# Performance work log

Measured on AMD Instinct MI355X. Metric: run time of the kernel, lower is better.

The kernel has to match this reference:

```python
import jax, jax.numpy as jnp
import numpy as np

EPS = 1e-12  # torch F.normalize eps


def setup_inputs() -> dict:
    key = jax.random.key(0)
    k1, k2, k3 = jax.random.split(key, 3)
    B, C, N, E, EMB = 128, 16, 128, 4, 16
    OUT = EMB // E  # Linear(emb_sz, emb_sz // num_edges)
    x = jax.random.normal(k1, (B, C, N, EMB), dtype=jnp.float32)
    A = jax.random.uniform(k2, (E, N, N), dtype=jnp.float32)  # non-negative adjacency
    # per-edge-type Linear weights, stored [E, in, out] so y = x @ W[e]
    W = jax.random.normal(k3, (E, EMB, OUT), dtype=jnp.float32) * (1.0 / np.sqrt(EMB))
    return {"x": x, "A": A, "W": W}


def reference(x, A, W):
    # F.normalize(A[e], dim=0): L2-normalize each column -> norm over rows (axis=1 of [E,N,N])
    col_norm = jnp.sqrt(jnp.sum(A * A, axis=1, keepdims=True))  # [E,1,N]
    An = A / jnp.maximum(col_norm, EPS)                         # [E,N,N]
    # x.transpose(3,2) @ An[e] then transpose back:
    # out[e,b,c,m,f] = sum_n x[b,c,n,f] * An[e,n,m]
    msg = jnp.einsum('bcnf,enm->ebcmf', x, An)                  # [E,B,C,N,EMB]
    # per-edge Linear (bias=False) + relu
    h = jax.nn.relu(jnp.einsum('ebcmf,efo->ebcmo', msg, W))     # [E,B,C,N,OUT]
    E_, B, C, N, O = h.shape
    # torch.cat([h_0, h_1, ...], axis=1) -> [B, E*C, N, OUT]
    out = jnp.transpose(h, (1, 0, 2, 3, 4)).reshape(B, E_ * C, N, O)
    return out
```

## Files before the change

### kernel.cpp

```cpp
#include <hip/hip_runtime.h>
#include <math.h>

#define EPSN 1e-12f

typedef __attribute__((ext_vector_type(8))) __bf16 bf16x8;
typedef __attribute__((ext_vector_type(8))) short short8;
typedef __attribute__((ext_vector_type(4))) float floatx4;

static __device__ __forceinline__ unsigned short f2bf(float f) {
    return __builtin_bit_cast(unsigned short, (__bf16)f);
}

__global__ __launch_bounds__(256)
void prep_kernel(const float* __restrict__ A, unsigned short* __restrict__ At) {
    __shared__ float Asub[128][33];
    __shared__ float red[8][32];
    __shared__ float rnv[32];
    const int t  = threadIdx.x;
    const int e  = blockIdx.x >> 2;
    const int m0 = (blockIdx.x & 3) * 32;
    const float* Ae = A + e * 16384 + m0;

    #pragma unroll
    for (int i = 0; i < 16; ++i) {
        int idx = t + i * 256;
        int n = idx >> 5, ml = idx & 31;
        Asub[n][ml] = Ae[n * 128 + ml];
    }
    __syncthreads();
    {
        int ml = t & 31, g = t >> 5;
        float s = 0.f;
        #pragma unroll
        for (int j = 0; j < 16; ++j) {
            float v = Asub[g * 16 + j][ml];
            s += v * v;
        }
        red[g][ml] = s;
    }
    __syncthreads();
    if (t < 32) {
        float s = 0.f;
        #pragma unroll
        for (int g = 0; g < 8; ++g) s += red[g][t];
        rnv[t] = 1.0f / fmaxf(sqrtf(s), EPSN);
    }
    __syncthreads();
    {
        int ml = t >> 3;
        int n0 = (t & 7) * 16;
        float r = rnv[ml];
        unsigned short hs[16];
        #pragma unroll
        for (int j = 0; j < 16; ++j)
            hs[j] = f2bf(Asub[n0 + j][ml] * r);
        uint4* dst = (uint4*)(At + ((size_t)(e * 128 + m0 + ml) * 128 + n0));
        dst[0] = *(const uint4*)&hs[0];
        dst[1] = *(const uint4*)&hs[8];
    }
}

__global__ __launch_bounds__(256, 4)
void gcn_mfma_kernel(const float* __restrict__ x, const float* __restrict__ W,
                     const unsigned short* __restrict__ At,
                     float* __restrict__ out) {
    __shared__ __align__(16) unsigned char xw[32768];

    const int t   = threadIdx.x;
    const int gid = blockIdx.x;
    const int h   = gid >> 8;
    const int bc0 = (gid & 255) * 8;

    float4 xf[4][4];
    #pragma unroll
    for (int p = 0; p < 4; ++p) {
        int pair = p * 256 + t;
        int bcl = pair >> 7, n = pair & 127;
        const float4* xp = (const float4*)(x + ((size_t)(bc0 + bcl) * 128 + n) * 16);
        xf[p][0] = xp[0]; xf[p][1] = xp[1]; xf[p][2] = xp[2]; xf[p][3] = xp[3];
    }
    const int nn = t & 127;
    #pragma unroll 1
    for (int e = 0; e < 4; ++e) {
        float4 We[16];
        const float4* wp = (const float4*)(W + e * 64);
        #pragma unroll
        for (int f = 0; f < 16; ++f) We[f] = wp[f];
        #pragma unroll
        for (int p = 0; p < 4; ++p) {
            float a0 = 0.f, a1 = 0.f, a2 = 0.f, a3 = 0.f;
            #pragma unroll
            for (int f = 0; f < 16; ++f) {
                float xv = ((const float*)&xf[p][f >> 2])[f & 3];
                a0 += xv * We[f].x; a1 += xv * We[f].y;
                a2 += xv * We[f].z; a3 += xv * We[f].w;
            }
            float av[4] = {a0, a1, a2, a3};
            int bcl = p * 2 + (t >> 7);
            #pragma unroll
            for (int o = 0; o < 4; ++o) {
                int r = bcl * 4 + o;
                int byteoff = (((e * 32 + r) << 8) + (nn << 1)) ^ ((r & 7) << 4);
                *(unsigned short*)(xw + byteoff) = f2bf(av[o]);
            }
        }
    }
    __syncthreads();

    const int e  = t >> 6;
    const int l  = t & 63;
    const int lr = l & 15;
    const int lg = l >> 4;

    bf16x8 afrag[2][4];
    #pragma unroll
    for (int rt = 0; rt < 2; ++rt) {
        #pragma unroll
        for (int ks = 0; ks < 4; ++ks) {
            int row = rt * 16 + lr;
            int n0 = ks * 32 + lg * 8;
            int byteoff = (((e * 32 + row) << 8) + (n0 << 1)) ^ ((row & 7) << 4);
            afrag[rt][ks] = __builtin_bit_cast(bf16x8, *(const short8*)(xw + byteoff));
        }
    }

    floatx4 acc[2][4];
    #pragma unroll
    for (int rt = 0; rt < 2; ++rt)
        #pragma unroll
        for (int mt = 0; mt < 4; ++mt)
            acc[rt][mt] = (floatx4){0.f, 0.f, 0.f, 0.f};

    const unsigned short* Ate = At + (size_t)e * 16384 + (size_t)h * 64 * 128;
    #pragma unroll
    for (int mt = 0; mt < 4; ++mt) {
        int m = mt * 16 + lr;
        bf16x8 bfrag[4];
        #pragma unroll
        for (int ks = 0; ks < 4; ++ks) {
            short8 v = *(const short8*)(Ate + (size_t)m * 128 + ks * 32 + lg * 8);
            bfrag[ks] = __builtin_bit_cast(bf16x8, v);
        }
        #pragma unroll
        for (int ks = 0; ks < 4; ++ks) {
            acc[0][mt] = __builtin_amdgcn_mfma_f32_16x16x32_bf16(
                afrag[0][ks], bfrag[ks], acc[0][mt], 0, 0, 0);
            acc[1][mt] = __builtin_amdgcn_mfma_f32_16x16x32_bf16(
                afrag[1][ks], bfrag[ks], acc[1][mt], 0, 0, 0);
        }
    }

    #pragma unroll
    for (int rt = 0; rt < 2; ++rt) {
        int bc = bc0 + rt * 4 + lg;
        int b = bc >> 4, c = bc & 15;
        float4* outp = (float4*)out + ((size_t)(b * 64 + e * 16 + c) * 128) + h * 64;
        #pragma unroll
        for (int mt = 0; mt < 4; ++mt) {
            float4 o4;
            o4.x = fmaxf(acc[rt][mt][0], 0.f);
            o4.y = fmaxf(acc[rt][mt][1], 0.f);
            o4.z = fmaxf(acc[rt][mt][2], 0.f);
            o4.w = fmaxf(acc[rt][mt][3], 0.f);
            outp[mt * 16 + lr] = o4;
        }
    }
}

extern "C" void kernel_launch(void* const* d_in, const int* in_sizes, int n_in,
                              void* d_out, int out_size, void* d_ws, size_t ws_size,
                              hipStream_t stream) {
    const float* x = (const float*)d_in[0];
    const float* A = (const float*)d_in[1];
    const float* W = (const float*)d_in[2];
    float* out = (float*)d_out;
    unsigned short* At = (unsigned short*)d_ws;

    prep_kernel<<<16, 256, 0, stream>>>(A, At);
    gcn_mfma_kernel<<<512, 256, 0, stream>>>(x, W, At, out);
}
```

Baseline: 21.38 us.

## Use MFMA for per-edge W projection and defer column normalization to epilogue

Replaces the scalar FMA x·W projection in the main kernel with a single bf16 MFMA per 16-row tile, converting x to bf16 on load, and adjusts the LDS swizzle to include the edge index. Prep is split into 68 blocks: 64 transpose-and-convert tiles of raw A, plus 4 blocks that compute inverse column norms, which the main kernel applies as a per-column scale before ReLU. The goals are to cut the VALU-heavy projection phase and to spread the serial prep kernel across more CUs. In exchange, x·W is now rounded to bf16 before the projection and unnormalized A is stored in bf16, and the norm blocks read A with strided column loads.

```diff
diff --git a/kernel.cpp b/kernel.cpp
--- a/kernel.cpp
+++ b/kernel.cpp
@@ -12,57 +12,43 @@
 }
 
 __global__ __launch_bounds__(256)
-void prep_kernel(const float* __restrict__ A, unsigned short* __restrict__ At) {
-    __shared__ float Asub[128][33];
-    __shared__ float red[8][32];
-    __shared__ float rnv[32];
-    const int t  = threadIdx.x;
-    const int e  = blockIdx.x >> 2;
-    const int m0 = (blockIdx.x & 3) * 32;
-    const float* Ae = A + e * 16384 + m0;
-
-    #pragma unroll
-    for (int i = 0; i < 16; ++i) {
-        int idx = t + i * 256;
-        int n = idx >> 5, ml = idx & 31;
-        Asub[n][ml] = Ae[n * 128 + ml];
-    }
-    __syncthreads();
-    {
-        int ml = t & 31, g = t >> 5;
-        float s = 0.f;
+void prep_kernel(const float* __restrict__ A, unsigned short* __restrict__ At,
+                 float* __restrict__ rnorm) {
+    __shared__ float Als[32][33];
+    const int t = threadIdx.x, bid = blockIdx.x;
+    if (bid < 64) {
+        const int e  = bid >> 4;
+        const int n0 = ((bid >> 2) & 3) * 32;
+        const int m0 = (bid & 3) * 32;
+        const float* Ae = A + e * 16384;
         #pragma unroll
-        for (int j = 0; j < 16; ++j) {
-            float v = Asub[g * 16 + j][ml];
-            s += v * v;
+        for (int i = 0; i < 4; ++i) {
+            int nl = i * 8 + (t >> 5), ml = t & 31;
+            Als[nl][ml] = Ae[(n0 + nl) * 128 + m0 + ml];
         }
-        red[g][ml] = s;
-    }
-    __syncthreads();
-    if (t < 32) {
-        float s = 0.f;
+        __syncthreads();
+        int ml = t >> 3, nc = (t & 7) * 4;
+        unsigned short hs[4] __attribute__((aligned(8)));
         #pragma unroll
-        for (int g = 0; g < 8; ++g) s += red[g][t];
-        rnv[t] = 1.0f / fmaxf(sqrtf(s), EPSN);
-    }
-    __syncthreads();
-    {
-        int ml = t >> 3;
-        int n0 = (t & 7) * 16;
-        float r = rnv[ml];
-        unsigned short hs[16];
-        #pragma unroll
-        for (int j = 0; j < 16; ++j)
-            hs[j] = f2bf(Asub[n0 + j][ml] * r);
-        uint4* dst = (uint4*)(At + ((size_t)(e * 128 + m0 + ml) * 128 + n0));
-        dst[0] = *(const uint4*)&hs[0];
-        dst[1] = *(const uint4*)&hs[8];
+        for (int j = 0; j < 4; ++j) hs[j] = f2bf(Als[nc + j][ml]);
+        *(unsigned long long*)(At + ((size_t)(e * 128 + m0 + ml) * 128 + n0 + nc)) =
+            *(const unsigned long long*)hs;
+    } else {
+        const int e = bid - 64;
+        if (t < 128) {
+            const float* Ae = A + e * 16384 + t;
+            float s = 0.f;
+            #pragma unroll 8
+            for (int n = 0; n < 128; ++n) { float v = Ae[n * 128]; s += v * v; }
+            rnorm[e * 128 + t] = 1.0f / fmaxf(sqrtf(s), EPSN);
+        }
     }
 }
 
 __global__ __launch_bounds__(256, 4)
 void gcn_mfma_kernel(const float* __restrict__ x, const float* __restrict__ W,
                      const unsigned short* __restrict__ At,
+                     const float* __restrict__ rnorm,
                      float* __restrict__ out) {
     __shared__ __align__(16) unsigned char xw[32768];
 
@@ -70,57 +56,65 @@
     const int gid = blockIdx.x;
     const int h   = gid >> 8;
     const int bc0 = (gid & 255) * 8;
+    const int wv  = t >> 6;
+    const int l   = t & 63;
+    const int cl  = l & 15;
+    const int lg  = l >> 4;
 
-    float4 xf[4][4];
+    bf16x8 bW;
+    {
+        short8 z = {0, 0, 0, 0, 0, 0, 0, 0};
+        bW = __builtin_bit_cast(bf16x8, z);
+        if (lg < 2) {
+            int eW = cl >> 2, oW = cl & 3;
+            unsigned short hs[8] __attribute__((aligned(16)));
+            #pragma unroll
+            for (int j = 0; j < 8; ++j)
+                hs[j] = f2bf(W[eW * 64 + (lg * 8 + j) * 4 + oW]);
+            bW = __builtin_bit_cast(bf16x8, *(const short8*)hs);
+        }
+    }
+
     #pragma unroll
-    for (int p = 0; p < 4; ++p) {
-        int pair = p * 256 + t;
-        int bcl = pair >> 7, n = pair & 127;
-        const float4* xp = (const float4*)(x + ((size_t)(bc0 + bcl) * 128 + n) * 16);
-        xf[p][0] = xp[0]; xf[p][1] = xp[1]; xf[p][2] = xp[2]; xf[p][3] = xp[3];
-    }
-    const int nn = t & 127;
-    #pragma unroll 1
-    for (int e = 0; e < 4; ++e) {
-        float4 We[16];
-        const float4* wp = (const float4*)(W + e * 64);
+    for (int ti = 0; ti < 16; ++ti) {
+        bf16x8 ax;
+        { short8 z = {0, 0, 0, 0, 0, 0, 0, 0}; ax = __builtin_bit_cast(bf16x8, z); }
+        if (lg < 2) {
+            int g = wv * 256 + ti * 16 + cl;
+            const float* xp = x + ((size_t)(bc0 + (g >> 7)) * 128 + (g & 127)) * 16 + lg * 8;
+            float4 v0 = *(const float4*)xp;
+            float4 v1 = *(const float4*)(xp + 4);
+            unsigned short hs[8] __attribute__((aligned(16)));
+            hs[0] = f2bf(v0.x); hs[1] = f2bf(v0.y); hs[2] = f2bf(v0.z); hs[3] = f2bf(v0.w);
+            hs[4] = f2bf(v1.x); hs[5] = f2bf(v1.y); hs[6] = f2bf(v1.z); hs[7] = f2bf(v1.w);
+            ax = __builtin_bit_cast(bf16x8, *(const short8*)hs);
+        }
+        floatx4 d = {0.f, 0.f, 0.f, 0.f};
+        d = __builtin_amdgcn_mfma_f32_16x16x32_bf16(ax, bW, d, 0, 0, 0);
+        int eD = cl >> 2, oD = cl & 3;
+        int rr = (wv * 2 + (ti >> 3)) * 4 + oD;
+        int nb = (ti & 7) * 16 + lg * 4;
+        int base = (eD * 32 + rr) << 8;
+        int s = (((rr & 7) ^ (eD << 1)) & 7) << 4;
         #pragma unroll
-        for (int f = 0; f < 16; ++f) We[f] = wp[f];
-        #pragma unroll
-        for (int p = 0; p < 4; ++p) {
-            float a0 = 0.f, a1 = 0.f, a2 = 0.f, a3 = 0.f;
-            #pragma unroll
-            for (int f = 0; f < 16; ++f) {
-                float xv = ((const float*)&xf[p][f >> 2])[f & 3];
-                a0 += xv * We[f].x; a1 += xv * We[f].y;
-                a2 += xv * We[f].z; a3 += xv * We[f].w;
-            }
-            float av[4] = {a0, a1, a2, a3};
-            int bcl = p * 2 + (t >> 7);
-            #pragma unroll
-            for (int o = 0; o < 4; ++o) {
-                int r = bcl * 4 + o;
-                int byteoff = (((e * 32 + r) << 8) + (nn << 1)) ^ ((r & 7) << 4);
-                *(unsigned short*)(xw + byteoff) = f2bf(av[o]);
-            }
+        for (int reg = 0; reg < 4; ++reg) {
+            int byteoff = (base + (nb + reg) * 2) ^ s;
+            *(unsigned short*)(xw + byteoff) = f2bf(d[reg]);
         }
     }
     __syncthreads();
 
-    const int e  = t >> 6;
-    const int l  = t & 63;
-    const int lr = l & 15;
-    const int lg = l >> 4;
-
-    bf16x8 afrag[2][4];
+    const int e = wv;
+    bf16x8 af[2][4];
     #pragma unroll
     for (int rt = 0; rt < 2; ++rt) {
         #pragma unroll
         for (int ks = 0; ks < 4; ++ks) {
-            int row = rt * 16 + lr;
+            int row = rt * 16 + cl;
             int n0 = ks * 32 + lg * 8;
-            int byteoff = (((e * 32 + row) << 8) + (n0 << 1)) ^ ((row & 7) << 4);
-            afrag[rt][ks] = __builtin_bit_cast(bf16x8, *(const short8*)(xw + byteoff));
+            int byteoff = (((e * 32 + row) << 8) + n0 * 2) ^
+                          ((((row & 7) ^ (e << 1)) & 7) << 4);
+            af[rt][ks] = __builtin_bit_cast(bf16x8, *(const short8*)(xw + byteoff));
         }
     }
 
@@ -134,22 +128,25 @@
     const unsigned short* Ate = At + (size_t)e * 16384 + (size_t)h * 64 * 128;
     #pragma unroll
     for (int mt = 0; mt < 4; ++mt) {
-        int m = mt * 16 + lr;
-        bf16x8 bfrag[4];
+        int m = mt * 16 + cl;
+        bf16x8 bfr[4];
         #pragma unroll
-        for (int ks = 0; ks < 4; ++ks) {
-            short8 v = *(const short8*)(Ate + (size_t)m * 128 + ks * 32 + lg * 8);
-            bfrag[ks] = __builtin_bit_cast(bf16x8, v);
-        }
+        for (int ks = 0; ks < 4; ++ks)
+            bfr[ks] = __builtin_bit_cast(bf16x8,
+                *(const short8*)(Ate + (size_t)m * 128 + ks * 32 + lg * 8));
         #pragma unroll
         for (int ks = 0; ks < 4; ++ks) {
             acc[0][mt] = __builtin_amdgcn_mfma_f32_16x16x32_bf16(
-                afrag[0][ks], bfrag[ks], acc[0][mt], 0, 0, 0);
+                af[0][ks], bfr[ks], acc[0][mt], 0, 0, 0);
             acc[1][mt] = __builtin_amdgcn_mfma_f32_16x16x32_bf16(
-                afrag[1][ks], bfrag[ks], acc[1][mt], 0, 0, 0);
+                af[1][ks], bfr[ks], acc[1][mt], 0, 0, 0);
         }
     }
 
+    float rnv[4];
+    #pragma unroll
+    for (int mt = 0; mt < 4; ++mt)
+        rnv[mt] = rnorm[e * 128 + h * 64 + mt * 16 + cl];
     #pragma unroll
     for (int rt = 0; rt < 2; ++rt) {
         int bc = bc0 + rt * 4 + lg;
@@ -157,12 +154,13 @@
         float4* outp = (float4*)out + ((size_t)(b * 64 + e * 16 + c) * 128) + h * 64;
         #pragma unroll
         for (int mt = 0; mt < 4; ++mt) {
+            float rn = rnv[mt];
             float4 o4;
-            o4.x = fmaxf(acc[rt][mt][0], 0.f);
-            o4.y = fmaxf(acc[rt][mt][1], 0.f);
-            o4.z = fmaxf(acc[rt][mt][2], 0.f);
-            o4.w = fmaxf(acc[rt][mt][3], 0.f);
-            outp[mt * 16 + lr] = o4;
+            o4.x = fmaxf(acc[rt][mt][0] * rn, 0.f);
+            o4.y = fmaxf(acc[rt][mt][1] * rn, 0.f);
+            o4.z = fmaxf(acc[rt][mt][2] * rn, 0.f);
+            o4.w = fmaxf(acc[rt][mt][3] * rn, 0.f);
+            outp[mt * 16 + cl] = o4;
         }
     }
 }
@@ -175,7 +173,8 @@
     const float* W = (const float*)d_in[2];
     float* out = (float*)d_out;
     unsigned short* At = (unsigned short*)d_ws;
+    float* rnorm = (float*)((char*)d_ws + 131072);
 
-    prep_kernel<<<16, 256, 0, stream>>>(A, At);
-    gcn_mfma_kernel<<<512, 256, 0, stream>>>(x, W, At, out);
+    prep_kernel<<<68, 256, 0, stream>>>(A, At, rnorm);
+    gcn_mfma_kernel<<<512, 256, 0, stream>>>(x, W, At, rnorm, out);
 }
```

Result: slower. 24.26 us (+13.5%).

## Fuse adjacency normalization into main kernel and apply column scale post-MFMA

Applied to the files above, without the earlier changes.

Drops the separate prep kernel. Each block now loads its 64-column slice of A for every edge type, transposes it to bf16 in shared memory, and accumulates column sums of squares. The normalization factor is applied to the MFMA accumulators before the relu, so A is quantized to bf16 without being normalized first. The per-edge loop now runs in all four waves, which adds two block barriers per edge, repeats the strided A loads in every block, and lowers occupancy (launch bounds 2, more LDS). The intent is to remove the second launch and the global round trip for the transposed A.

```diff
diff --git a/kernel.cpp b/kernel.cpp
--- a/kernel.cpp
+++ b/kernel.cpp
@@ -11,65 +11,25 @@
     return __builtin_bit_cast(unsigned short, (__bf16)f);
 }
 
-__global__ __launch_bounds__(256)
-void prep_kernel(const float* __restrict__ A, unsigned short* __restrict__ At) {
-    __shared__ float Asub[128][33];
-    __shared__ float red[8][32];
-    __shared__ float rnv[32];
-    const int t  = threadIdx.x;
-    const int e  = blockIdx.x >> 2;
-    const int m0 = (blockIdx.x & 3) * 32;
-    const float* Ae = A + e * 16384 + m0;
-
-    #pragma unroll
-    for (int i = 0; i < 16; ++i) {
-        int idx = t + i * 256;
-        int n = idx >> 5, ml = idx & 31;
-        Asub[n][ml] = Ae[n * 128 + ml];
-    }
-    __syncthreads();
-    {
-        int ml = t & 31, g = t >> 5;
-        float s = 0.f;
-        #pragma unroll
-        for (int j = 0; j < 16; ++j) {
-            float v = Asub[g * 16 + j][ml];
-            s += v * v;
-        }
-        red[g][ml] = s;
-    }
-    __syncthreads();
-    if (t < 32) {
-        float s = 0.f;
-        #pragma unroll
-        for (int g = 0; g < 8; ++g) s += red[g][t];
-        rnv[t] = 1.0f / fmaxf(sqrtf(s), EPSN);
-    }
-    __syncthreads();
-    {
-        int ml = t >> 3;
-        int n0 = (t & 7) * 16;
-        float r = rnv[ml];
-        unsigned short hs[16];
-        #pragma unroll
-        for (int j = 0; j < 16; ++j)
-            hs[j] = f2bf(Asub[n0 + j][ml] * r);
-        uint4* dst = (uint4*)(At + ((size_t)(e * 128 + m0 + ml) * 128 + n0));
-        dst[0] = *(const uint4*)&hs[0];
-        dst[1] = *(const uint4*)&hs[8];
-    }
-}
-
-__global__ __launch_bounds__(256, 4)
-void gcn_mfma_kernel(const float* __restrict__ x, const float* __restrict__ W,
-                     const unsigned short* __restrict__ At,
-                     float* __restrict__ out) {
+__global__ __launch_bounds__(256, 2)
+void gcn_fused(const float* __restrict__ x, const float* __restrict__ A,
+               const float* __restrict__ W, float* __restrict__ out) {
     __shared__ __align__(16) unsigned char xw[32768];
+    __shared__ __align__(16) unsigned char at[16384];
+    __shared__ float red[4][64];
 
     const int t   = threadIdx.x;
     const int gid = blockIdx.x;
     const int h   = gid >> 8;
     const int bc0 = (gid & 255) * 8;
+    const int m0  = h * 64;
+
+    const int w  = t >> 6;
+    const int l  = t & 63;
+    const int cl = l & 15;
+    const int lg = l >> 4;
+    const int ml = t & 63;
+    const int ng = t >> 6;
 
     float4 xf[4][4];
     #pragma unroll
@@ -79,90 +39,102 @@
         const float4* xp = (const float4*)(x + ((size_t)(bc0 + bcl) * 128 + n) * 16);
         xf[p][0] = xp[0]; xf[p][1] = xp[1]; xf[p][2] = xp[2]; xf[p][3] = xp[3];
     }
-    const int nn = t & 127;
+
+    auto transpose_step = [&](int e) {
+        const float* Ae = A + e * 16384 + m0 + ml;
+        float ssq = 0.f;
+        #pragma unroll
+        for (int it = 0; it < 4; ++it) {
+            int n0 = it * 32 + ng * 8;
+            float v[8];
+            #pragma unroll
+            for (int j = 0; j < 8; ++j) v[j] = Ae[(size_t)(n0 + j) * 128];
+            unsigned short hs[8] __attribute__((aligned(16)));
+            #pragma unroll
+            for (int j = 0; j < 8; ++j) { ssq += v[j] * v[j]; hs[j] = f2bf(v[j]); }
+            int byteoff = ((ml << 8) + n0 * 2) ^ ((ml & 7) << 4);
+            *(short8*)(at + byteoff) = *(const short8*)hs;
+        }
+        red[ng][ml] = ssq;
+    };
+
+    transpose_step(0);
+
     #pragma unroll 1
     for (int e = 0; e < 4; ++e) {
-        float4 We[16];
-        const float4* wp = (const float4*)(W + e * 64);
-        #pragma unroll
-        for (int f = 0; f < 16; ++f) We[f] = wp[f];
+        const float* We = W + e * 64;
         #pragma unroll
         for (int p = 0; p < 4; ++p) {
+            int bcl = p * 2 + (t >> 7);
+            int n   = t & 127;
             float a0 = 0.f, a1 = 0.f, a2 = 0.f, a3 = 0.f;
             #pragma unroll
             for (int f = 0; f < 16; ++f) {
                 float xv = ((const float*)&xf[p][f >> 2])[f & 3];
-                a0 += xv * We[f].x; a1 += xv * We[f].y;
-                a2 += xv * We[f].z; a3 += xv * We[f].w;
+                a0 += xv * We[f * 4 + 0];
+                a1 += xv * We[f * 4 + 1];
+                a2 += xv * We[f * 4 + 2];
+                a3 += xv * We[f * 4 + 3];
             }
             float av[4] = {a0, a1, a2, a3};
-            int bcl = p * 2 + (t >> 7);
             #pragma unroll
             for (int o = 0; o < 4; ++o) {
                 int r = bcl * 4 + o;
-                int byteoff = (((e * 32 + r) << 8) + (nn << 1)) ^ ((r & 7) << 4);
+                int byteoff = (((e * 32 + r) << 8) + n * 2) ^ ((r & 7) << 4);
                 *(unsigned short*)(xw + byteoff) = f2bf(av[o]);
             }
         }
     }
     __syncthreads();
 
-    const int e  = t >> 6;
-    const int l  = t & 63;
-    const int lr = l & 15;
-    const int lg = l >> 4;
-
-    bf16x8 afrag[2][4];
-    #pragma unroll
-    for (int rt = 0; rt < 2; ++rt) {
+    #pragma unroll 1
+    for (int e = 0; e < 4; ++e) {
+        bf16x8 af[2][4];
+        #pragma unroll
+        for (int rt = 0; rt < 2; ++rt)
+            #pragma unroll
+            for (int ks = 0; ks < 4; ++ks) {
+                int row = rt * 16 + cl;
+                int byteoff = (((e * 32 + row) << 8) + (ks * 32 + lg * 8) * 2)
+                              ^ ((row & 7) << 4);
+                af[rt][ks] = __builtin_bit_cast(bf16x8, *(const short8*)(xw + byteoff));
+            }
+        const int mrow = w * 16 + cl;
+        bf16x8 bfr[4];
         #pragma unroll
         for (int ks = 0; ks < 4; ++ks) {
-            int row = rt * 16 + lr;
-            int n0 = ks * 32 + lg * 8;
-            int byteoff = (((e * 32 + row) << 8) + (n0 << 1)) ^ ((row & 7) << 4);
-            afrag[rt][ks] = __builtin_bit_cast(bf16x8, *(const short8*)(xw + byteoff));
+            int byteoff = ((mrow << 8) + (ks * 32 + lg * 8) * 2) ^ ((mrow & 7) << 4);
+            bfr[ks] = __builtin_bit_cast(bf16x8, *(const short8*)(at + byteoff));
         }
-    }
 
-    floatx4 acc[2][4];
-    #pragma unroll
-    for (int rt = 0; rt < 2; ++rt)
-        #pragma unroll
-        for (int mt = 0; mt < 4; ++mt)
-            acc[rt][mt] = (floatx4){0.f, 0.f, 0.f, 0.f};
-
-    const unsigned short* Ate = At + (size_t)e * 16384 + (size_t)h * 64 * 128;
-    #pragma unroll
-    for (int mt = 0; mt < 4; ++mt) {
-        int m = mt * 16 + lr;
-        bf16x8 bfrag[4];
+        floatx4 acc0 = {0.f, 0.f, 0.f, 0.f};
+        floatx4 acc1 = {0.f, 0.f, 0.f, 0.f};
         #pragma unroll
         for (int ks = 0; ks < 4; ++ks) {
-            short8 v = *(const short8*)(Ate + (size_t)m * 128 + ks * 32 + lg * 8);
-            bfrag[ks] = __builtin_bit_cast(bf16x8, v);
+            acc0 = __builtin_amdgcn_mfma_f32_16x16x32_bf16(af[0][ks], bfr[ks], acc0, 0, 0, 0);
+            acc1 = __builtin_amdgcn_mfma_f32_16x16x32_bf16(af[1][ks], bfr[ks], acc1, 0, 0, 0);
         }
+
+        float s = red[0][mrow] + red[1][mrow] + red[2][mrow] + red[3][mrow];
+        float rn = 1.0f / fmaxf(sqrtf(s), EPSN);
+
         #pragma unroll
-        for (int ks = 0; ks < 4; ++ks) {
-            acc[0][mt] = __builtin_amdgcn_mfma_f32_16x16x32_bf16(
-                afrag[0][ks], bfrag[ks], acc[0][mt], 0, 0, 0);
-            acc[1][mt] = __builtin_amdgcn_mfma_f32_16x16x32_bf16(
-                afrag[1][ks], bfrag[ks], acc[1][mt], 0, 0, 0);
+        for (int rt = 0; rt < 2; ++rt) {
+            floatx4 a = rt ? acc1 : acc0;
+            int bc = bc0 + rt * 4 + lg;
+            int b = bc >> 4, c = bc & 15;
+            float4 o4;
+            o4.x = fmaxf(a[0] * rn, 0.f);
+            o4.y = fmaxf(a[1] * rn, 0.f);
+            o4.z = fmaxf(a[2] * rn, 0.f);
+            o4.w = fmaxf(a[3] * rn, 0.f);
+            ((float4*)out)[(size_t)(b * 64 + e * 16 + c) * 128 + m0 + mrow] = o4;
         }
-    }
 
-    #pragma unroll
-    for (int rt = 0; rt < 2; ++rt) {
-        int bc = bc0 + rt * 4 + lg;
-        int b = bc >> 4, c = bc & 15;
-        float4* outp = (float4*)out + ((size_t)(b * 64 + e * 16 + c) * 128) + h * 64;
-        #pragma unroll
-        for (int mt = 0; mt < 4; ++mt) {
-            float4 o4;
-            o4.x = fmaxf(acc[rt][mt][0], 0.f);
-            o4.y = fmaxf(acc[rt][mt][1], 0.f);
-            o4.z = fmaxf(acc[rt][mt][2], 0.f);
-            o4.w = fmaxf(acc[rt][mt][3], 0.f);
-            outp[mt * 16 + lr] = o4;
+        if (e < 3) {
+            __syncthreads();
+            transpose_step(e + 1);
+            __syncthreads();
         }
     }
 }
@@ -174,8 +146,6 @@
     const float* A = (const float*)d_in[1];
     const float* W = (const float*)d_in[2];
     float* out = (float*)d_out;
-    unsigned short* At = (unsigned short*)d_ws;
 
-    prep_kernel<<<16, 256, 0, stream>>>(A, At);
-    gcn_mfma_kernel<<<512, 256, 0, stream>>>(x, W, At, out);
+    gcn_fused<<<512, 256, 0, stream>>>(x, A, W, out);
 }
```

Measured after the change: 24.28 us. 1.14x slower.
